# Kernel optimization log

Hardware: AMD Instinct MI355X
Metric: run time of the kernel (lower is better)

Reference implementation:

```python
import jax, jax.numpy as jnp
import numpy as np

N_NODES = 100000


def _sage_conv(x, edge_index, W_l, b_l, W_r):
    # PyG SAGEConv (aggr='mean', root_weight=True):
    #   out = lin_l(mean_{j in N(i)} x_j) + lin_r(x_i)
    src, dst = edge_index[0], edge_index[1]
    msg = x[src]                                            # [E, C] gather
    agg = jax.ops.segment_sum(msg, dst, num_segments=N_NODES)  # [N, C]
    deg = jax.ops.segment_sum(jnp.ones((edge_index.shape[1],), x.dtype), dst,
                              num_segments=N_NODES)
    agg = agg / jnp.maximum(deg, 1.0)[:, None]              # mean aggregation
    return agg @ W_l + b_l + x @ W_r


def setup_inputs() -> dict:
    key = jax.random.key(0)
    ks = jax.random.split(key, 10)
    d, h = 128, 128
    s = 1.0 / np.sqrt(d)
    x = jax.random.normal(ks[0], (N_NODES, d), dtype=jnp.float32)
    edge_index = jax.random.randint(ks[1], (2, 640000), 0, N_NODES, dtype=jnp.int64)
    return {
        "x": x,
        "edge_index": edge_index,
        "W1_l": jax.random.uniform(ks[2], (d, h), jnp.float32, -s, s),
        "b1": jnp.zeros((h,), jnp.float32),
        "W1_r": jax.random.uniform(ks[3], (d, h), jnp.float32, -s, s),
        "W2_l": jax.random.uniform(ks[4], (h, h), jnp.float32, -s, s),
        "b2": jnp.zeros((h,), jnp.float32),
        "W2_r": jax.random.uniform(ks[5], (h, h), jnp.float32, -s, s),
        "W_lin": jax.random.uniform(ks[6], (h, 1), jnp.float32, -s, s),
        "b_lin": jnp.zeros((1,), jnp.float32),
    }


def reference(x, edge_index, W1_l, b1, W1_r, W2_l, b2, W2_r, W_lin, b_lin):
    h = jax.nn.relu(_sage_conv(x, edge_index, W1_l, b1, W1_r))
    h = jax.nn.relu(_sage_conv(h, edge_index, W2_l, b2, W2_r))
    return h @ W_lin + b_lin  # [N, 1]
```

## Files before the change

kernel.cpp:

```cpp
#include <hip/hip_runtime.h>
#include <hip/hip_bf16.h>


#define ND 128
#define KTOT 256
#define CAP 32
#define TM 32
#define AGS 136

typedef __bf16 bf16x8 __attribute__((ext_vector_type(8)));
typedef float floatx16 __attribute__((ext_vector_type(16)));

__device__ inline unsigned short f2bf(float f) {
    union { float f; unsigned u; } v; v.f = f;
    unsigned r = v.u + 0x7fffu + ((v.u >> 16) & 1u);
    return (unsigned short)(r >> 16);
}
__device__ inline float bf_lo(unsigned u) { return __uint_as_float(u << 16); }
__device__ inline float bf_hi(unsigned u) { return __uint_as_float(u & 0xffff0000u); }

__global__ void k_prep_all(const float* __restrict__ x, unsigned short* __restrict__ xbf,
                           unsigned short* __restrict__ h1bf, int n,
                           int nElems,
                           const float* __restrict__ W1l, const float* __restrict__ W1r,
                           unsigned short* __restrict__ Wt1,
                           const float* __restrict__ W2l, const float* __restrict__ W2r,
                           unsigned short* __restrict__ Wt2,
                           const int* __restrict__ esrc_in, const int* __restrict__ edst_in,
                           int* __restrict__ cnt, int* __restrict__ ebuk, int E) {
    const int t = threadIdx.x;
    const int tid = blockIdx.x * 256 + t;

    const int e = blockIdx.x * 128 + t;
    const bool doE = (t < 128) && (e < E);
    int d0 = 0, s0 = 0;
    if (doE) {
        d0 = edst_in[e];
        s0 = esrc_in[e];
    }

    const int i = tid * 8;
    float4 xa, xc;
    const bool doX = (i < nElems);
    if (doX) {
        xa = *(const float4*)(x + i);
        xc = *(const float4*)(x + i + 4);
    }

    int p0 = -1;
    if (doE) p0 = atomicAdd(&cnt[d0], 1);

    if (doX) {
        uint4 r;
        r.x = (unsigned)f2bf(xa.x) | ((unsigned)f2bf(xa.y) << 16);
        r.y = (unsigned)f2bf(xa.z) | ((unsigned)f2bf(xa.w) << 16);
        r.z = (unsigned)f2bf(xc.x) | ((unsigned)f2bf(xc.y) << 16);
        r.w = (unsigned)f2bf(xc.z) | ((unsigned)f2bf(xc.w) << 16);
        *(uint4*)(xbf + i) = r;
    }

    if (tid < 32) {
        int4 z = {0, 0, 0, 0};
        unsigned short* zp = (tid < 16) ? xbf : h1bf;
        ((int4*)(zp + (size_t)n * ND))[tid & 15] = z;
    }

    if (tid < 2 * KTOT * ND) {
        const int half = tid >> 15;
        const int idx = tid & 32767;
        const int nn = idx >> 8;
        const int kk = idx & 255;
        const float* Wl = half ? W2l : W1l;
        const float* Wr = half ? W2r : W1r;
        unsigned short* Wt = half ? Wt2 : Wt1;
        float v = (kk < 128) ? Wl[(size_t)kk * ND + nn] : Wr[(size_t)(kk - 128) * ND + nn];
        const int n32 = nn >> 5, r = nn & 31;
        const int kc = kk >> 5, ks = (kk >> 4) & 1, lh = (kk >> 3) & 1, k8 = kk & 7;
        Wt[n32 * 8192 + kc * 1024 + ks * 512 + (lh * 32 + r) * 8 + k8] = f2bf(v);
    }

    if (p0 >= 0 && p0 < CAP) ebuk[d0 * CAP + p0] = s0;
}

__device__ __forceinline__ void gatherTM(const unsigned short* __restrict__ feat,
                                         const int* __restrict__ cnt,
                                         const int* __restrict__ ebuk,
                                         int n, int m0, int t,
                                         unsigned short* Agg) {
    const int l = t & 15;
    const int g = t >> 4;
#pragma unroll
    for (int p = 0; p < TM / 16; ++p) {
        const int nl = p * 16 + g;
        const int node = m0 + nl;
        int d = 0;
        if (node < n) d = cnt[node];
        const int dd = min(d, CAP);
        const int4* lst4 = (const int4*)(ebuk + (size_t)node * CAP);
        const int4 L0 = lst4[0];
        const int4 L1 = lst4[1];
        int s[8];
        s[0] = (0 < dd) ? L0.x : n;
        s[1] = (1 < dd) ? L0.y : n;
        s[2] = (2 < dd) ? L0.z : n;
        s[3] = (3 < dd) ? L0.w : n;
        s[4] = (4 < dd) ? L1.x : n;
        s[5] = (5 < dd) ? L1.y : n;
        s[6] = (6 < dd) ? L1.z : n;
        s[7] = (7 < dd) ? L1.w : n;
        uint4 v[8];
#pragma unroll
        for (int k = 0; k < 8; ++k)
            v[k] = ((const uint4*)(feat + (size_t)s[k] * ND))[l];
        float a[8] = {0.f, 0.f, 0.f, 0.f, 0.f, 0.f, 0.f, 0.f};
#pragma unroll
        for (int k = 0; k < 8; ++k) {
            a[0] += bf_lo(v[k].x); a[1] += bf_hi(v[k].x);
            a[2] += bf_lo(v[k].y); a[3] += bf_hi(v[k].y);
            a[4] += bf_lo(v[k].z); a[5] += bf_hi(v[k].z);
            a[6] += bf_lo(v[k].w); a[7] += bf_hi(v[k].w);
        }
        if (dd > 8) {
            for (int j = 8; j < dd; j += 8) {
                const int4 M0 = lst4[j >> 2];
                const int4 M1 = lst4[(j >> 2) + 1];
                int q[8];
                q[0] = (j + 0 < dd) ? M0.x : n;
                q[1] = (j + 1 < dd) ? M0.y : n;
                q[2] = (j + 2 < dd) ? M0.z : n;
                q[3] = (j + 3 < dd) ? M0.w : n;
                q[4] = (j + 4 < dd) ? M1.x : n;
                q[5] = (j + 5 < dd) ? M1.y : n;
                q[6] = (j + 6 < dd) ? M1.z : n;
                q[7] = (j + 7 < dd) ? M1.w : n;
                uint4 w[8];
#pragma unroll
                for (int k = 0; k < 8; ++k)
                    w[k] = ((const uint4*)(feat + (size_t)q[k] * ND))[l];
#pragma unroll
                for (int k = 0; k < 8; ++k) {
                    a[0] += bf_lo(w[k].x); a[1] += bf_hi(w[k].x);
                    a[2] += bf_lo(w[k].y); a[3] += bf_hi(w[k].y);
                    a[4] += bf_lo(w[k].z); a[5] += bf_hi(w[k].z);
                    a[6] += bf_lo(w[k].w); a[7] += bf_hi(w[k].w);
                }
            }
        }
        float inv = 1.0f / (float)max(d, 1);
        uint4 r;
        r.x = (unsigned)f2bf(a[0] * inv) | ((unsigned)f2bf(a[1] * inv) << 16);
        r.y = (unsigned)f2bf(a[2] * inv) | ((unsigned)f2bf(a[3] * inv) << 16);
        r.z = (unsigned)f2bf(a[4] * inv) | ((unsigned)f2bf(a[5] * inv) << 16);
        r.w = (unsigned)f2bf(a[6] * inv) | ((unsigned)f2bf(a[7] * inv) << 16);
        *(uint4*)&Agg[nl * AGS + l * 8] = r;
    }
}

__device__ __forceinline__ void stageSelf(const unsigned short* __restrict__ feat,
                                          int n, int m0, int t,
                                          unsigned short* Sf) {
#pragma unroll
    for (int q = 0; q < (TM * ND / 8) / 256; ++q) {
        const int idx = t + q * 256;
        const int row = idx >> 4;
        const int c16 = idx & 15;
        int4 w = {0, 0, 0, 0};
        const int gr = m0 + row;
        if (gr < n) w = *(const int4*)(feat + (size_t)gr * ND + c16 * 8);
        *(int4*)&Sf[row * AGS + c16 * 8] = w;
    }
}

__launch_bounds__(256, 6)
__global__ void k_layer1_fused(const unsigned short* __restrict__ feat,
                               const unsigned short* __restrict__ Wt,
                               const float* __restrict__ bias,
                               const int* __restrict__ cnt,
                               const int* __restrict__ ebuk,
                               unsigned short* __restrict__ out, int n) {
    __shared__ __align__(16) unsigned short Agg[TM * AGS];
    __shared__ __align__(16) unsigned short Sf[TM * AGS];
    const int t = threadIdx.x;
    const int m0 = blockIdx.x * TM;

    gatherTM(feat, cnt, ebuk, n, m0, t, Agg);
    stageSelf(feat, n, m0, t, Sf);
    __syncthreads();

    const int wave = t >> 6, lane = t & 63;
    const int l31 = lane & 31, lhalf = lane >> 5;
    const int wn = wave * 32;
    const unsigned short* Bw = Wt + wave * 8192;

    floatx16 acc = (floatx16)0.0f;

#pragma unroll
    for (int kc = 0; kc < 8; ++kc) {
        const unsigned short* Ab = (kc < 4)
            ? &Agg[l31 * AGS + kc * 32]
            : &Sf[l31 * AGS + (kc - 4) * 32];
        bf16x8 af[2], bfr[2];
#pragma unroll
        for (int ks = 0; ks < 2; ++ks) {
            af[ks]  = *(const bf16x8*)(Ab + ks * 16 + lhalf * 8);
            bfr[ks] = *(const bf16x8*)(Bw + kc * 1024 + ks * 512 + lane * 8);
        }
        acc = __builtin_amdgcn_mfma_f32_32x32x16_bf16(af[0], bfr[0], acc, 0, 0, 0);
        acc = __builtin_amdgcn_mfma_f32_32x32x16_bf16(af[1], bfr[1], acc, 0, 0, 0);
    }

    const int c = wn + l31;
    const float bv = bias[c];
#pragma unroll
    for (int reg = 0; reg < 16; ++reg) {
        const int row = m0 + lhalf * 4 + (reg & 3) + 8 * (reg >> 2);
        if (row < n) {
            float v = fmaxf(acc[reg] + bv, 0.f);
            out[(size_t)row * ND + c] = f2bf(v);
        }
    }
}

__launch_bounds__(256, 6)
__global__ void k_layer2_fused_head(const unsigned short* __restrict__ feat,
                                    const unsigned short* __restrict__ Wt,
                                    const float* __restrict__ bias,
                                    const float* __restrict__ Wlin,
                                    const float* __restrict__ blin,
                                    const int* __restrict__ cnt,
                                    const int* __restrict__ ebuk,
                                    float* __restrict__ out, int n) {
    __shared__ __align__(16) unsigned short Agg[TM * AGS];
    __shared__ __align__(16) unsigned short Sf[TM * AGS];
    __shared__ float part[TM][4];
    const int t = threadIdx.x;
    const int m0 = blockIdx.x * TM;

    gatherTM(feat, cnt, ebuk, n, m0, t, Agg);
    stageSelf(feat, n, m0, t, Sf);
    __syncthreads();

    const int wave = t >> 6, lane = t & 63;
    const int l31 = lane & 31, lhalf = lane >> 5;
    const int wn = wave * 32;
    const unsigned short* Bw = Wt + wave * 8192;

    floatx16 acc = (floatx16)0.0f;

#pragma unroll
    for (int kc = 0; kc < 8; ++kc) {
        const unsigned short* Ab = (kc < 4)
            ? &Agg[l31 * AGS + kc * 32]
            : &Sf[l31 * AGS + (kc - 4) * 32];
        bf16x8 af[2], bfr[2];
#pragma unroll
        for (int ks = 0; ks < 2; ++ks) {
            af[ks]  = *(const bf16x8*)(Ab + ks * 16 + lhalf * 8);
            bfr[ks] = *(const bf16x8*)(Bw + kc * 1024 + ks * 512 + lane * 8);
        }
        acc = __builtin_amdgcn_mfma_f32_32x32x16_bf16(af[0], bfr[0], acc, 0, 0, 0);
        acc = __builtin_amdgcn_mfma_f32_32x32x16_bf16(af[1], bfr[1], acc, 0, 0, 0);
    }

    const int c = wn + l31;
    const float bv = bias[c];
    const float wv = Wlin[c];
    float p[16];
#pragma unroll
    for (int reg = 0; reg < 16; ++reg)
        p[reg] = fmaxf(acc[reg] + bv, 0.f) * wv;
#pragma unroll
    for (int reg = 0; reg < 16; ++reg) {
        float v = p[reg];
        v += __shfl_xor(v, 1);
        v += __shfl_xor(v, 2);
        v += __shfl_xor(v, 4);
        v += __shfl_xor(v, 8);
        v += __shfl_xor(v, 16);
        if (l31 == 0) {
            int rl = lhalf * 4 + (reg & 3) + 8 * (reg >> 2);
            part[rl][wave] = v;
        }
    }
    __syncthreads();
    if (t < TM) {
        int row = m0 + t;
        if (row < n)
            out[row] = part[t][0] + part[t][1] + part[t][2] + part[t][3] + blin[0];
    }
}

extern "C" void kernel_launch(void* const* d_in, const int* in_sizes, int n_in,
                              void* d_out, int out_size, void* d_ws, size_t ws_size,
                              hipStream_t stream) {
    const float* x    = (const float*)d_in[0];
    const int*   edge = (const int*)d_in[1];
    const float* W1l  = (const float*)d_in[2];
    const float* b1   = (const float*)d_in[3];
    const float* W1r  = (const float*)d_in[4];
    const float* W2l  = (const float*)d_in[5];
    const float* b2   = (const float*)d_in[6];
    const float* W2r  = (const float*)d_in[7];
    const float* Wlin = (const float*)d_in[8];
    const float* blin = (const float*)d_in[9];
    float* out = (float*)d_out;

    int n = out_size;
    int E = in_sizes[1] / 2;
    (void)n_in; (void)ws_size;

    char* ws = (char*)d_ws;
    size_t off = 0;
    auto take = [&](size_t bytes) -> char* {
        char* p = ws + off;
        off += (bytes + 255) & ~(size_t)255;
        return p;
    };
    int* cnt    = (int*)take((size_t)n * 4);
    int* ebuk   = (int*)take((size_t)n * CAP * 4);
    unsigned short* xbf  = (unsigned short*)take((size_t)(n + 1) * ND * 2);
    unsigned short* h1bf = (unsigned short*)take((size_t)(n + 1) * ND * 2);
    unsigned short* Wt1  = (unsigned short*)take((size_t)ND * KTOT * 2);
    unsigned short* Wt2  = (unsigned short*)take((size_t)ND * KTOT * 2);

    hipMemsetAsync(cnt, 0, (size_t)n * 4, stream);

    const int* esrc_in = edge;
    const int* edst_in = edge + E;

    int nElems = n * ND;
    int prepBlocks = (nElems / 8 + 255) / 256;

    k_prep_all<<<prepBlocks, 256, 0, stream>>>(
        x, xbf, h1bf, n, nElems, W1l, W1r, Wt1, W2l, W2r, Wt2,
        esrc_in, edst_in, cnt, ebuk, E);

    int gemmBlocks = (n + TM - 1) / TM;

    k_layer1_fused<<<gemmBlocks, 256, 0, stream>>>(xbf, Wt1, b1, cnt, ebuk, h1bf, n);
    k_layer2_fused_head<<<gemmBlocks, 256, 0, stream>>>(h1bf, Wt2, b2, Wlin, blin, cnt, ebuk, out, n);
}
```

Before: 216.0 us.

## Merge memset, prep and both layers into one cooperative persistent kernel

Replaces the memset plus three kernel launches with a single cooperative kernel that uses grid-wide syncs between the zeroing, prep, layer-1 and layer-2 phases, striding over work with a persistent grid sized from occupancy (capped at 2048 blocks). The aim is to remove launch gaps and per-kernel tail effects. In exchange, grid.sync has its own cost, launch bounds drop from 6 to 4 waves, and the persistent loops add __syncthreads per tile. If the cooperative launch fails, it falls back to the old path.

```diff
diff --git a/kernel.cpp b/kernel.cpp
--- a/kernel.cpp
+++ b/kernel.cpp
@@ -1,5 +1,8 @@
 #include <hip/hip_runtime.h>
+#include <hip/hip_cooperative_groups.h>
 #include <hip/hip_bf16.h>
+
+namespace cg = cooperative_groups;
 
 
 #define ND 128
@@ -19,19 +22,18 @@
 __device__ inline float bf_lo(unsigned u) { return __uint_as_float(u << 16); }
 __device__ inline float bf_hi(unsigned u) { return __uint_as_float(u & 0xffff0000u); }
 
-__global__ void k_prep_all(const float* __restrict__ x, unsigned short* __restrict__ xbf,
-                           unsigned short* __restrict__ h1bf, int n,
-                           int nElems,
+__device__ __forceinline__ void prep_chunk(int c, int t,
+                           const float* __restrict__ x, unsigned short* __restrict__ xbf,
+                           unsigned short* __restrict__ h1bf, int n, int nElems,
                            const float* __restrict__ W1l, const float* __restrict__ W1r,
                            unsigned short* __restrict__ Wt1,
                            const float* __restrict__ W2l, const float* __restrict__ W2r,
                            unsigned short* __restrict__ Wt2,
                            const int* __restrict__ esrc_in, const int* __restrict__ edst_in,
                            int* __restrict__ cnt, int* __restrict__ ebuk, int E) {
-    const int t = threadIdx.x;
-    const int tid = blockIdx.x * 256 + t;
-
-    const int e = blockIdx.x * 128 + t;
+    const int tid = c * 256 + t;
+
+    const int e = c * 128 + t;
     const bool doE = (t < 128) && (e < E);
     int d0 = 0, s0 = 0;
     if (doE) {
@@ -171,6 +173,151 @@
     }
 }
 
+__device__ __forceinline__ floatx16 gemm32(const unsigned short* Agg, const unsigned short* Sf,
+                                           const unsigned short* __restrict__ Wt,
+                                           int wave, int lane) {
+    const int l31 = lane & 31, lhalf = lane >> 5;
+    const unsigned short* Bw = Wt + wave * 8192;
+    floatx16 acc = (floatx16)0.0f;
+#pragma unroll
+    for (int kc = 0; kc < 8; ++kc) {
+        const unsigned short* Ab = (kc < 4)
+            ? &Agg[l31 * AGS + kc * 32]
+            : &Sf[l31 * AGS + (kc - 4) * 32];
+        bf16x8 af0 = *(const bf16x8*)(Ab + lhalf * 8);
+        bf16x8 af1 = *(const bf16x8*)(Ab + 16 + lhalf * 8);
+        bf16x8 bf0 = *(const bf16x8*)(Wt + wave * 8192 + kc * 1024 + lane * 8);
+        bf16x8 bf1 = *(const bf16x8*)(Wt + wave * 8192 + kc * 1024 + 512 + lane * 8);
+        (void)Bw;
+        acc = __builtin_amdgcn_mfma_f32_32x32x16_bf16(af0, bf0, acc, 0, 0, 0);
+        acc = __builtin_amdgcn_mfma_f32_32x32x16_bf16(af1, bf1, acc, 0, 0, 0);
+    }
+    return acc;
+}
+
+__device__ __forceinline__ void l1_tile(const unsigned short* __restrict__ feat,
+                                        const unsigned short* __restrict__ Wt,
+                                        const float* __restrict__ bias,
+                                        const int* __restrict__ cnt,
+                                        const int* __restrict__ ebuk,
+                                        unsigned short* __restrict__ out,
+                                        int n, int m0, int t,
+                                        unsigned short* Agg, unsigned short* Sf) {
+    gatherTM(feat, cnt, ebuk, n, m0, t, Agg);
+    stageSelf(feat, n, m0, t, Sf);
+    __syncthreads();
+    const int wave = t >> 6, lane = t & 63;
+    const int l31 = lane & 31, lhalf = lane >> 5;
+    floatx16 acc = gemm32(Agg, Sf, Wt, wave, lane);
+    const int c = wave * 32 + l31;
+    const float bv = bias[c];
+#pragma unroll
+    for (int reg = 0; reg < 16; ++reg) {
+        const int row = m0 + lhalf * 4 + (reg & 3) + 8 * (reg >> 2);
+        if (row < n) {
+            float v = fmaxf(acc[reg] + bv, 0.f);
+            out[(size_t)row * ND + c] = f2bf(v);
+        }
+    }
+    __syncthreads();
+}
+
+__device__ __forceinline__ void l2h_tile(const unsigned short* __restrict__ feat,
+                                         const unsigned short* __restrict__ Wt,
+                                         const float* __restrict__ bias,
+                                         const float* __restrict__ Wlin,
+                                         const float* __restrict__ blin,
+                                         const int* __restrict__ cnt,
+                                         const int* __restrict__ ebuk,
+                                         float* __restrict__ out,
+                                         int n, int m0, int t,
+                                         unsigned short* Agg, unsigned short* Sf,
+                                         float (*part)[4]) {
+    gatherTM(feat, cnt, ebuk, n, m0, t, Agg);
+    stageSelf(feat, n, m0, t, Sf);
+    __syncthreads();
+    const int wave = t >> 6, lane = t & 63;
+    const int l31 = lane & 31, lhalf = lane >> 5;
+    floatx16 acc = gemm32(Agg, Sf, Wt, wave, lane);
+    const int c = wave * 32 + l31;
+    const float bv = bias[c];
+    const float wv = Wlin[c];
+    float p[16];
+#pragma unroll
+    for (int reg = 0; reg < 16; ++reg)
+        p[reg] = fmaxf(acc[reg] + bv, 0.f) * wv;
+#pragma unroll
+    for (int reg = 0; reg < 16; ++reg) {
+        float v = p[reg];
+        v += __shfl_xor(v, 1);
+        v += __shfl_xor(v, 2);
+        v += __shfl_xor(v, 4);
+        v += __shfl_xor(v, 8);
+        v += __shfl_xor(v, 16);
+        if (l31 == 0) {
+            int rl = lhalf * 4 + (reg & 3) + 8 * (reg >> 2);
+            part[rl][wave] = v;
+        }
+    }
+    __syncthreads();
+    if (t < TM) {
+        int row = m0 + t;
+        if (row < n)
+            out[row] = part[t][0] + part[t][1] + part[t][2] + part[t][3] + blin[0];
+    }
+    __syncthreads();
+}
+
+__launch_bounds__(256, 4)
+__global__ void k_mega(const float* __restrict__ x,
+                       unsigned short* __restrict__ xbf,
+                       unsigned short* __restrict__ h1bf,
+                       int n, int nElems, int nPrepChunks, int nTiles,
+                       const float* __restrict__ W1l, const float* __restrict__ W1r,
+                       unsigned short* __restrict__ Wt1,
+                       const float* __restrict__ W2l, const float* __restrict__ W2r,
+                       unsigned short* __restrict__ Wt2,
+                       const float* __restrict__ b1, const float* __restrict__ b2,
+                       const float* __restrict__ Wlin, const float* __restrict__ blin,
+                       const int* __restrict__ esrc, const int* __restrict__ edst,
+                       int* __restrict__ cnt, int* __restrict__ ebuk, int E,
+                       float* __restrict__ out) {
+    cg::grid_group grid = cg::this_grid();
+    __shared__ __align__(16) unsigned short Agg[TM * AGS];
+    __shared__ __align__(16) unsigned short Sf[TM * AGS];
+    __shared__ float part[TM][4];
+    const int t = threadIdx.x;
+    const int b = blockIdx.x;
+    const int G = gridDim.x;
+
+    for (int i = b * 256 + t; i < n; i += G * 256) cnt[i] = 0;
+    grid.sync();
+
+    for (int c = b; c < nPrepChunks; c += G)
+        prep_chunk(c, t, x, xbf, h1bf, n, nElems, W1l, W1r, Wt1, W2l, W2r, Wt2,
+                   esrc, edst, cnt, ebuk, E);
+    grid.sync();
+
+    for (int tile = b; tile < nTiles; tile += G)
+        l1_tile(xbf, Wt1, b1, cnt, ebuk, h1bf, n, tile * TM, t, Agg, Sf);
+    grid.sync();
+
+    for (int tile = b; tile < nTiles; tile += G)
+        l2h_tile(h1bf, Wt2, b2, Wlin, blin, cnt, ebuk, out, n, tile * TM, t, Agg, Sf, part);
+}
+
+__global__ void k_prep_all(const float* __restrict__ x, unsigned short* __restrict__ xbf,
+                           unsigned short* __restrict__ h1bf, int n, int nElems,
+                           const float* __restrict__ W1l, const float* __restrict__ W1r,
+                           unsigned short* __restrict__ Wt1,
+                           const float* __restrict__ W2l, const float* __restrict__ W2r,
+                           unsigned short* __restrict__ Wt2,
+                           const int* __restrict__ esrc_in, const int* __restrict__ edst_in,
+                           int* __restrict__ cnt, int* __restrict__ ebuk, int E) {
+    prep_chunk(blockIdx.x, threadIdx.x, x, xbf, h1bf, n, nElems,
+               W1l, W1r, Wt1, W2l, W2r, Wt2, esrc_in, edst_in, cnt, ebuk, E);
+}
+
 __launch_bounds__(256, 6)
 __global__ void k_layer1_fused(const unsigned short* __restrict__ feat,
                                const unsigned short* __restrict__ Wt,
@@ -180,45 +327,7 @@
                                unsigned short* __restrict__ out, int n) {
     __shared__ __align__(16) unsigned short Agg[TM * AGS];
     __shared__ __align__(16) unsigned short Sf[TM * AGS];
-    const int t = threadIdx.x;
-    const int m0 = blockIdx.x * TM;
-
-    gatherTM(feat, cnt, ebuk, n, m0, t, Agg);
-    stageSelf(feat, n, m0, t, Sf);
-    __syncthreads();
-
-    const int wave = t >> 6, lane = t & 63;
-    const int l31 = lane & 31, lhalf = lane >> 5;
-    const int wn = wave * 32;
-    const unsigned short* Bw = Wt + wave * 8192;
-
-    floatx16 acc = (floatx16)0.0f;
-
-#pragma unroll
-    for (int kc = 0; kc < 8; ++kc) {
-        const unsigned short* Ab = (kc < 4)
-            ? &Agg[l31 * AGS + kc * 32]
-            : &Sf[l31 * AGS + (kc - 4) * 32];
-        bf16x8 af[2], bfr[2];
-#pragma unroll
-        for (int ks = 0; ks < 2; ++ks) {
-            af[ks]  = *(const bf16x8*)(Ab + ks * 16 + lhalf * 8);
-            bfr[ks] = *(const bf16x8*)(Bw + kc * 1024 + ks * 512 + lane * 8);
-        }
-        acc = __builtin_amdgcn_mfma_f32_32x32x16_bf16(af[0], bfr[0], acc, 0, 0, 0);
-        acc = __builtin_amdgcn_mfma_f32_32x32x16_bf16(af[1], bfr[1], acc, 0, 0, 0);
-    }
-
-    const int c = wn + l31;
-    const float bv = bias[c];
-#pragma unroll
-    for (int reg = 0; reg < 16; ++reg) {
-        const int row = m0 + lhalf * 4 + (reg & 3) + 8 * (reg >> 2);
-        if (row < n) {
-            float v = fmaxf(acc[reg] + bv, 0.f);
-            out[(size_t)row * ND + c] = f2bf(v);
-        }
-    }
+    l1_tile(feat, Wt, bias, cnt, ebuk, out, n, blockIdx.x * TM, threadIdx.x, Agg, Sf);
 }
 
 __launch_bounds__(256, 6)
@@ -233,61 +342,8 @@
     __shared__ __align__(16) unsigned short Agg[TM * AGS];
     __shared__ __align__(16) unsigned short Sf[TM * AGS];
     __shared__ float part[TM][4];
-    const int t = threadIdx.x;
-    const int m0 = blockIdx.x * TM;
-
-    gatherTM(feat, cnt, ebuk, n, m0, t, Agg);
-    stageSelf(feat, n, m0, t, Sf);
-    __syncthreads();
-
-    const int wave = t >> 6, lane = t & 63;
-    const int l31 = lane & 31, lhalf = lane >> 5;
-    const int wn = wave * 32;
-    const unsigned short* Bw = Wt + wave * 8192;
-
-    floatx16 acc = (floatx16)0.0f;
-
-#pragma unroll
-    for (int kc = 0; kc < 8; ++kc) {
-        const unsigned short* Ab = (kc < 4)
-            ? &Agg[l31 * AGS + kc * 32]
-            : &Sf[l31 * AGS + (kc - 4) * 32];
-        bf16x8 af[2], bfr[2];
-#pragma unroll
-        for (int ks = 0; ks < 2; ++ks) {
-            af[ks]  = *(const bf16x8*)(Ab + ks * 16 + lhalf * 8);
-            bfr[ks] = *(const bf16x8*)(Bw + kc * 1024 + ks * 512 + lane * 8);
-        }
-        acc = __builtin_amdgcn_mfma_f32_32x32x16_bf16(af[0], bfr[0], acc, 0, 0, 0);
-        acc = __builtin_amdgcn_mfma_f32_32x32x16_bf16(af[1], bfr[1], acc, 0, 0, 0);
-    }
-
-    const int c = wn + l31;
-    const float bv = bias[c];
-    const float wv = Wlin[c];
-    float p[16];
-#pragma unroll
-    for (int reg = 0; reg < 16; ++reg)
-        p[reg] = fmaxf(acc[reg] + bv, 0.f) * wv;
-#pragma unroll
-    for (int reg = 0; reg < 16; ++reg) {
-        float v = p[reg];
-        v += __shfl_xor(v, 1);
-        v += __shfl_xor(v, 2);
-        v += __shfl_xor(v, 4);
-        v += __shfl_xor(v, 8);
-        v += __shfl_xor(v, 16);
-        if (l31 == 0) {
-            int rl = lhalf * 4 + (reg & 3) + 8 * (reg >> 2);
-            part[rl][wave] = v;
-        }
-    }
-    __syncthreads();
-    if (t < TM) {
-        int row = m0 + t;
-        if (row < n)
-            out[row] = part[t][0] + part[t][1] + part[t][2] + part[t][3] + blin[0];
-    }
+    l2h_tile(feat, Wt, bias, Wlin, blin, cnt, ebuk, out, n, blockIdx.x * TM, threadIdx.x,
+             Agg, Sf, part);
 }
 
 extern "C" void kernel_launch(void* const* d_in, const int* in_sizes, int n_in,
@@ -323,20 +379,41 @@
     unsigned short* Wt1  = (unsigned short*)take((size_t)ND * KTOT * 2);
     unsigned short* Wt2  = (unsigned short*)take((size_t)ND * KTOT * 2);
 
+    const int* esrc = edge;
+    const int* edst = edge + E;
+
+    int nElems = n * ND;
+    int nPrepChunks = (nElems / 8 + 255) / 256;
+    int nTiles = (n + TM - 1) / TM;
+
+    static int blocksPerCU = 0;
+    if (blocksPerCU == 0) {
+        int nb = 0;
+        if (hipOccupancyMaxActiveBlocksPerMultiprocessor(&nb, (const void*)k_mega, 256, 0)
+                != hipSuccess || nb <= 0)
+            nb = 4;
+        blocksPerCU = nb;
+    }
+    int G = blocksPerCU * 256;
+    if (G > 2048) G = 2048;
+
+    void* args[] = { (void*)&x, (void*)&xbf, (void*)&h1bf, (void*)&n, (void*)&nElems,
+                     (void*)&nPrepChunks, (void*)&nTiles,
+                     (void*)&W1l, (void*)&W1r, (void*)&Wt1,
+                     (void*)&W2l, (void*)&W2r, (void*)&Wt2,
+                     (void*)&b1, (void*)&b2, (void*)&Wlin, (void*)&blin,
+                     (void*)&esrc, (void*)&edst, (void*)&cnt, (void*)&ebuk,
+                     (void*)&E, (void*)&out };
+
+    hipError_t rc = hipLaunchCooperativeKernel((const void*)k_mega, dim3(G), dim3(256),
+                                               args, 0, stream);
+    if (rc == hipSuccess) return;
+
     hipMemsetAsync(cnt, 0, (size_t)n * 4, stream);
-
-    const int* esrc_in = edge;
-    const int* edst_in = edge + E;
-
-    int nElems = n * ND;
-    int prepBlocks = (nElems / 8 + 255) / 256;
-
+    int prepBlocks = nPrepChunks;
     k_prep_all<<<prepBlocks, 256, 0, stream>>>(
         x, xbf, h1bf, n, nElems, W1l, W1r, Wt1, W2l, W2r, Wt2,
-        esrc_in, edst_in, cnt, ebuk, E);
-
-    int gemmBlocks = (n + TM - 1) / TM;
-
-    k_layer1_fused<<<gemmBlocks, 256, 0, stream>>>(xbf, Wt1, b1, cnt, ebuk, h1bf, n);
-    k_layer2_fused_head<<<gemmBlocks, 256, 0, stream>>>(h1bf, Wt2, b2, Wlin, blin, cnt, ebuk, out, n);
-}
+        esrc, edst, cnt, ebuk, E);
+    k_layer1_fused<<<nTiles, 256, 0, stream>>>(xbf, Wt1, b1, cnt, ebuk, h1bf, n);
+    k_layer2_fused_head<<<nTiles, 256, 0, stream>>>(h1bf, Wt2, b2, Wlin, blin, cnt, ebuk, out, n);
+}
```

After: 429.4 us. +98.8%, slower.
